# Kernel tuning notes

Measured on AMD Instinct MI355X. Metric: run time of the kernel, lower is better.

## Reference

```python
import jax, jax.numpy as jnp
import numpy as np


def setup_inputs() -> dict:
    key = jax.random.key(0)
    kx, kw = jax.random.split(key)
    B, IN, OUT = 8192, 1024, 4096
    x = jax.random.normal(kx, (B, IN), dtype=jnp.float32)
    # torch.rand -> uniform [0,1)
    weight = jax.random.uniform(kw, (IN, OUT), dtype=jnp.float32)
    return {"x": x, "weight": weight}


def reference(x, weight):
    # Faithful to: (x.unsqueeze(-1) - weight).pow(2).sum(-2)
    # i.e. out[b, o] = sum_i (x[b, i] - weight[i, o])**2
    # Computed via the squared-distance expansion to avoid the
    # (B, in, out) broadcast intermediate:
    x_sq = jnp.sum(x * x, axis=-1, keepdims=True)          # (B, 1)
    w_sq = jnp.sum(weight * weight, axis=0)                # (OUT,)
    cross = jnp.matmul(x, weight)                          # (B, OUT)
    return x_sq - 2.0 * cross + w_sq
```

## Files before the change

kernel.cpp:

```cpp
#include <hip/hip_runtime.h>
#include <cstdint>
#include <cstddef>

#define B_DIM   8192
#define IN_DIM  1024
#define OUT_DIM 4096
#define KT2     (IN_DIM / 64)

typedef __attribute__((ext_vector_type(8)))  int   i32x8;
typedef __attribute__((ext_vector_type(4)))  int   i32x4;
typedef __attribute__((ext_vector_type(16))) float f32x16;

__device__ __forceinline__ void async_copy16(const void* gptr, void* ldsptr) {
    __builtin_amdgcn_global_load_lds(
        (__attribute__((address_space(1))) void*)gptr,
        (__attribute__((address_space(3))) void*)ldsptr,
        16, 0, 0);
}

__device__ __forceinline__ int pack4_fp8(float a, float b, float c, float d) {
    int pk = __builtin_amdgcn_cvt_pk_fp8_f32(a, b, 0, false);
    pk = __builtin_amdgcn_cvt_pk_fp8_f32(c, d, pk, true);
    return pk;
}


__global__ __launch_bounds__(512) void tile_x_kernel(
    const float* __restrict__ x, unsigned char* __restrict__ At,
    float* __restrict__ xsq, float* __restrict__ wsq)
{
    const int t = threadIdx.x;
    const int w = t >> 6;
    const int l = t & 63;
    const int mt = blockIdx.x;
    const int m  = mt * 32 + (l & 31);

    float s = 0.0f;
    #pragma unroll
    for (int c = 0; c < 2; ++c) {
        const int kt2 = c * 8 + w;
        const float* src = x + (size_t)m * IN_DIM + kt2 * 64 + (l >> 5) * 32;
        i32x4 lo, hi;
        #pragma unroll
        for (int j = 0; j < 4; ++j) {
            float4 v = ((const float4*)src)[j];
            s += v.x*v.x + v.y*v.y + v.z*v.z + v.w*v.w;
            lo[j] = pack4_fp8(v.x, v.y, v.z, v.w);
        }
        #pragma unroll
        for (int j = 0; j < 4; ++j) {
            float4 v = ((const float4*)src)[4 + j];
            s += v.x*v.x + v.y*v.y + v.z*v.z + v.w*v.w;
            hi[j] = pack4_fp8(v.x, v.y, v.z, v.w);
        }
        unsigned char* pan = At + ((size_t)mt * KT2 + kt2) * 2048;
        *(i32x4*)(pan + l * 16)        = lo;
        *(i32x4*)(pan + 1024 + l * 16) = hi;
    }
    s += __shfl_down(s, 32, 64);
    __shared__ float red[8][32];
    if (l < 32) red[w][l] = s;
    __syncthreads();
    if (t < 32) {
        float r = 0.0f;
        #pragma unroll
        for (int j = 0; j < 8; ++j) r += red[j][t];
        xsq[mt * 32 + t] = r;
    }

    if (blockIdx.x < 8) wsq[blockIdx.x * 512 + t] = 0.0f;
}

__global__ __launch_bounds__(256) void tile_w_kernel(
    const float* __restrict__ wgt, unsigned char* __restrict__ Bt,
    float* __restrict__ wsq)
{
    __shared__ float tile[256 * 33];
    const int t  = threadIdx.x;
    const int w  = t >> 6;
    const int l  = t & 63;
    const int nt = blockIdx.x;
    const int q  = blockIdx.y;
    const int n0 = nt * 32;

    {
        const int rbase = t >> 2, cg = (t & 3) * 8;
        #pragma unroll
        for (int rep = 0; rep < 4; ++rep) {
            const int r = rbase + rep * 64;
            const float* src = wgt + (size_t)(q * 256 + r) * OUT_DIM + n0 + cg;
            float4 v0 = ((const float4*)src)[0];
            float4 v1 = ((const float4*)src)[1];
            float* d = &tile[r * 33 + cg];
            d[0] = v0.x; d[1] = v0.y; d[2] = v0.z; d[3] = v0.w;
            d[4] = v1.x; d[5] = v1.y; d[6] = v1.z; d[7] = v1.w;
        }
    }
    __syncthreads();

    const int kt2 = q * 4 + w;
    const int n   = l & 31;
    const int kb  = w * 64 + (l >> 5) * 32;
    float s = 0.0f;
    i32x4 lo, hi;
    #pragma unroll
    for (int j4 = 0; j4 < 4; ++j4) {
        float f0 = tile[(kb + j4 * 4 + 0) * 33 + n];
        float f1 = tile[(kb + j4 * 4 + 1) * 33 + n];
        float f2 = tile[(kb + j4 * 4 + 2) * 33 + n];
        float f3 = tile[(kb + j4 * 4 + 3) * 33 + n];
        s += f0*f0 + f1*f1 + f2*f2 + f3*f3;
        lo[j4] = pack4_fp8(f0, f1, f2, f3);
    }
    #pragma unroll
    for (int j4 = 0; j4 < 4; ++j4) {
        float f0 = tile[(kb + 16 + j4 * 4 + 0) * 33 + n];
        float f1 = tile[(kb + 16 + j4 * 4 + 1) * 33 + n];
        float f2 = tile[(kb + 16 + j4 * 4 + 2) * 33 + n];
        float f3 = tile[(kb + 16 + j4 * 4 + 3) * 33 + n];
        s += f0*f0 + f1*f1 + f2*f2 + f3*f3;
        hi[j4] = pack4_fp8(f0, f1, f2, f3);
    }
    unsigned char* pan = Bt + ((size_t)nt * KT2 + kt2) * 2048;
    *(i32x4*)(pan + l * 16)        = lo;
    *(i32x4*)(pan + 1024 + l * 16) = hi;

    s += __shfl_down(s, 32, 64);
    __shared__ float red[4][32];
    if (l < 32) red[w][l] = s;
    __syncthreads();
    if (t < 32) atomicAdd(&wsq[n0 + t], red[0][t] + red[1][t] + red[2][t] + red[3][t]);
}

__global__ __launch_bounds__(256, 2) void rbf_gemm_kernel(
    const unsigned char* __restrict__ At,
    const unsigned char* __restrict__ Bt,
    const float* __restrict__ xsq,
    const float* __restrict__ wsq,
    float* __restrict__ out)
{
    __shared__ __align__(16) unsigned char sm[73728];

    const int t    = threadIdx.x;
    const int w    = t >> 6;
    const int l    = t & 63;
    const int l32  = l & 31;
    const int half = l >> 5;

    const int wg  = blockIdx.y * 64 + blockIdx.x;
    const int swz = (wg & 7) * 128 + (wg >> 3);
    const int bm  = swz >> 4;
    const int bn  = swz & 15;

    f32x16 acc[4][2];
    #pragma unroll
    for (int mi = 0; mi < 4; ++mi)
        #pragma unroll
        for (int ni = 0; ni < 2; ++ni)
            #pragma unroll
            for (int r = 0; r < 16; ++r)
                acc[mi][ni][r] = 0.0f;

    const unsigned char* gaBase  = At + (size_t)(bm * 4 + w)      * (KT2 * 2048);
    const unsigned char* gbBase0 = Bt + (size_t)(bn * 8 + w * 2)  * (KT2 * 2048);
    const unsigned char* gbBase1 = gbBase0 + (size_t)(KT2 * 2048);

    auto stage = [&](int buf, int k) {
        unsigned char* As = sm + buf * 24576;
        unsigned char* Bs = As + 8192;
        const unsigned char* ga  = gaBase  + k * 2048;
        const unsigned char* gb0 = gbBase0 + k * 2048;
        const unsigned char* gb1 = gbBase1 + k * 2048;
        #pragma unroll
        for (int h = 0; h < 2; ++h) {
            async_copy16(ga  + h * 1024 + l * 16, As + w * 2048 + h * 1024);
            async_copy16(gb0 + h * 1024 + l * 16, Bs + (w * 2 + 0) * 2048 + h * 1024);
            async_copy16(gb1 + h * 1024 + l * 16, Bs + (w * 2 + 1) * 2048 + h * 1024);
        }
    };

    auto ldfrag = [&](const unsigned char* base, int p) -> i32x8 {
        i32x4 lo = *(const i32x4*)(base + p * 2048 + l * 16);
        i32x4 hi = *(const i32x4*)(base + p * 2048 + 1024 + l * 16);
        i32x8 r;
        r[0] = lo[0]; r[1] = lo[1]; r[2] = lo[2]; r[3] = lo[3];
        r[4] = hi[0]; r[5] = hi[1]; r[6] = hi[2]; r[7] = hi[3];
        return r;
    };

    stage(0, 0);
    stage(1, 1);

    int cb = 0, sb = 2;
    for (int k = 0; k < 16; ++k) {
        if (k < 15) asm volatile("s_waitcnt vmcnt(6)" ::: "memory");
        else        asm volatile("s_waitcnt vmcnt(0)" ::: "memory");
        __builtin_amdgcn_s_barrier();
        __builtin_amdgcn_sched_barrier(0);

        if (k <= 13) stage(sb, k + 2);

        const unsigned char* As = sm + cb * 24576;
        const unsigned char* Bs = As + 8192;
        i32x8 bf0 = ldfrag(Bs, w * 2 + 0);
        i32x8 bf1 = ldfrag(Bs, w * 2 + 1);
        i32x8 af[4];
        #pragma unroll
        for (int mi = 0; mi < 4; ++mi)
            af[mi] = ldfrag(As, mi);

        __builtin_amdgcn_s_setprio(1);
        #pragma unroll
        for (int mi = 0; mi < 4; ++mi) {
            acc[mi][0] = __builtin_amdgcn_mfma_scale_f32_32x32x64_f8f6f4(
                af[mi], bf0, acc[mi][0],
                0, 0,
                0, 0x7F7F7F7F,
                0, 0x7F7F7F7F);
            acc[mi][1] = __builtin_amdgcn_mfma_scale_f32_32x32x64_f8f6f4(
                af[mi], bf1, acc[mi][1],
                0, 0, 0, 0x7F7F7F7F, 0, 0x7F7F7F7F);
        }
        __builtin_amdgcn_s_setprio(0);

        cb = (cb == 2) ? 0 : cb + 1;
        sb = (sb == 2) ? 0 : sb + 1;
    }

    const int ncol = bn * 256 + w * 64 + l32;
    const float wsn0 = wsq[ncol];
    const float wsn1 = wsq[ncol + 32];
    #pragma unroll
    for (int mi = 0; mi < 4; ++mi) {
        const int mbase = bm * 128 + mi * 32 + 4 * half;
        #pragma unroll
        for (int r2 = 0; r2 < 4; ++r2) {
            #pragma unroll
            for (int r1 = 0; r1 < 4; ++r1) {
                const int m  = mbase + r1 + 8 * r2;
                const float xs = xsq[m];
                float* orow = out + (size_t)m * OUT_DIM + ncol;
                orow[0]  = xs + wsn0 - 2.0f * acc[mi][0][r2 * 4 + r1];
                orow[32] = xs + wsn1 - 2.0f * acc[mi][1][r2 * 4 + r1];
            }
        }
    }
}

extern "C" void kernel_launch(void* const* d_in, const int* in_sizes, int n_in,
                              void* d_out, int out_size, void* d_ws, size_t ws_size,
                              hipStream_t stream)
{
    const float* x   = (const float*)d_in[0];
    const float* wgt = (const float*)d_in[1];
    float* out = (float*)d_out;
    char*  ws  = (char*)d_ws;

    unsigned char* At = (unsigned char*)ws;
    unsigned char* Bt = (unsigned char*)(ws + (size_t)B_DIM * IN_DIM);
    float* xsq = (float*)(ws + (size_t)B_DIM * IN_DIM + (size_t)OUT_DIM * IN_DIM);
    float* wsq = xsq + B_DIM;

    tile_x_kernel<<<B_DIM / 32, 512, 0, stream>>>(x, At, xsq, wsq);
    tile_w_kernel<<<dim3(OUT_DIM / 32, 4), 256, 0, stream>>>(wgt, Bt, wsq);
    rbf_gemm_kernel<<<dim3(64, 16), 256, 0, stream>>>(At, Bt, xsq, wsq, out);
}
```

Before: 194.4 us.

## Merge x and weight quantization kernels and replace atomics with partial sums

Combines the two preprocessing kernels into one launch of 1024 blocks. The first 512 blocks quantize x and the rest quantize the weight. The atomicAdd on the weight norms, and the zeroing it needed, are replaced by per-quarter partial sums that the GEMM epilogue adds up, along with two partial sums for the x norms. This saves one kernel launch and the atomic traffic, and lets the two quantization jobs share the machine. In exchange the epilogue does a few extra loads, and the fused kernel needs the larger LDS tile for every block.

```diff
diff --git a/kernel.cpp b/kernel.cpp
--- a/kernel.cpp
+++ b/kernel.cpp
@@ -25,65 +25,55 @@
 }
 
 
-__global__ __launch_bounds__(512) void tile_x_kernel(
-    const float* __restrict__ x, unsigned char* __restrict__ At,
-    float* __restrict__ xsq, float* __restrict__ wsq)
+__global__ __launch_bounds__(256) void quant_kernel(
+    const float* __restrict__ x, const float* __restrict__ wgt,
+    unsigned char* __restrict__ At, unsigned char* __restrict__ Bt,
+    float* __restrict__ xsq2,
+    float* __restrict__ wsq2)
 {
+    __shared__ float tile[256 * 33];
+    __shared__ float red[4][32];
+
     const int t = threadIdx.x;
     const int w = t >> 6;
     const int l = t & 63;
-    const int mt = blockIdx.x;
-    const int m  = mt * 32 + (l & 31);
-
-    float s = 0.0f;
-    #pragma unroll
-    for (int c = 0; c < 2; ++c) {
-        const int kt2 = c * 8 + w;
-        const float* src = x + (size_t)m * IN_DIM + kt2 * 64 + (l >> 5) * 32;
-        i32x4 lo, hi;
-        #pragma unroll
-        for (int j = 0; j < 4; ++j) {
-            float4 v = ((const float4*)src)[j];
-            s += v.x*v.x + v.y*v.y + v.z*v.z + v.w*v.w;
-            lo[j] = pack4_fp8(v.x, v.y, v.z, v.w);
-        }
-        #pragma unroll
-        for (int j = 0; j < 4; ++j) {
-            float4 v = ((const float4*)src)[4 + j];
-            s += v.x*v.x + v.y*v.y + v.z*v.z + v.w*v.w;
-            hi[j] = pack4_fp8(v.x, v.y, v.z, v.w);
-        }
-        unsigned char* pan = At + ((size_t)mt * KT2 + kt2) * 2048;
-        *(i32x4*)(pan + l * 16)        = lo;
-        *(i32x4*)(pan + 1024 + l * 16) = hi;
-    }
-    s += __shfl_down(s, 32, 64);
-    __shared__ float red[8][32];
-    if (l < 32) red[w][l] = s;
-    __syncthreads();
-    if (t < 32) {
-        float r = 0.0f;
-        #pragma unroll
-        for (int j = 0; j < 8; ++j) r += red[j][t];
-        xsq[mt * 32 + t] = r;
-    }
-
-    if (blockIdx.x < 8) wsq[blockIdx.x * 512 + t] = 0.0f;
-}
-
-__global__ __launch_bounds__(256) void tile_w_kernel(
-    const float* __restrict__ wgt, unsigned char* __restrict__ Bt,
-    float* __restrict__ wsq)
-{
-    __shared__ float tile[256 * 33];
-    const int t  = threadIdx.x;
-    const int w  = t >> 6;
-    const int l  = t & 63;
-    const int nt = blockIdx.x;
-    const int q  = blockIdx.y;
-    const int n0 = nt * 32;
-
-    {
+    const int b = blockIdx.x;
+
+    if (b < 512) {
+        const int mt = b >> 1, kh = b & 1;
+        const int m  = mt * 32 + (l & 31);
+        float s = 0.0f;
+        #pragma unroll
+        for (int p = 0; p < 2; ++p) {
+            const int kt2 = kh * 8 + w * 2 + p;
+            const float* src = x + (size_t)m * IN_DIM + kt2 * 64 + (l >> 5) * 32;
+            i32x4 lo, hi;
+            #pragma unroll
+            for (int j = 0; j < 4; ++j) {
+                float4 v = ((const float4*)src)[j];
+                s += v.x*v.x + v.y*v.y + v.z*v.z + v.w*v.w;
+                lo[j] = pack4_fp8(v.x, v.y, v.z, v.w);
+            }
+            #pragma unroll
+            for (int j = 0; j < 4; ++j) {
+                float4 v = ((const float4*)src)[4 + j];
+                s += v.x*v.x + v.y*v.y + v.z*v.z + v.w*v.w;
+                hi[j] = pack4_fp8(v.x, v.y, v.z, v.w);
+            }
+            unsigned char* pan = At + ((size_t)mt * KT2 + kt2) * 2048;
+            *(i32x4*)(pan + l * 16)        = lo;
+            *(i32x4*)(pan + 1024 + l * 16) = hi;
+        }
+        s += __shfl_down(s, 32, 64);
+        if (l < 32) red[w][l] = s;
+        __syncthreads();
+        if (t < 32)
+            xsq2[kh * B_DIM + mt * 32 + t] =
+                red[0][t] + red[1][t] + red[2][t] + red[3][t];
+    } else {
+        const int idx = b - 512;
+        const int nt = idx & 127, q = idx >> 7, n0 = nt * 32;
+
         const int rbase = t >> 2, cg = (t & 3) * 8;
         #pragma unroll
         for (int rep = 0; rep < 4; ++rep) {
@@ -95,48 +85,49 @@
             d[0] = v0.x; d[1] = v0.y; d[2] = v0.z; d[3] = v0.w;
             d[4] = v1.x; d[5] = v1.y; d[6] = v1.z; d[7] = v1.w;
         }
+        __syncthreads();
+
+        const int kt2 = q * 4 + w;
+        const int n   = l & 31;
+        const int kb  = w * 64 + (l >> 5) * 32;
+        float s = 0.0f;
+        i32x4 lo, hi;
+        #pragma unroll
+        for (int j4 = 0; j4 < 4; ++j4) {
+            float f0 = tile[(kb + j4 * 4 + 0) * 33 + n];
+            float f1 = tile[(kb + j4 * 4 + 1) * 33 + n];
+            float f2 = tile[(kb + j4 * 4 + 2) * 33 + n];
+            float f3 = tile[(kb + j4 * 4 + 3) * 33 + n];
+            s += f0*f0 + f1*f1 + f2*f2 + f3*f3;
+            lo[j4] = pack4_fp8(f0, f1, f2, f3);
+        }
+        #pragma unroll
+        for (int j4 = 0; j4 < 4; ++j4) {
+            float f0 = tile[(kb + 16 + j4 * 4 + 0) * 33 + n];
+            float f1 = tile[(kb + 16 + j4 * 4 + 1) * 33 + n];
+            float f2 = tile[(kb + 16 + j4 * 4 + 2) * 33 + n];
+            float f3 = tile[(kb + 16 + j4 * 4 + 3) * 33 + n];
+            s += f0*f0 + f1*f1 + f2*f2 + f3*f3;
+            hi[j4] = pack4_fp8(f0, f1, f2, f3);
+        }
+        unsigned char* pan = Bt + ((size_t)nt * KT2 + kt2) * 2048;
+        *(i32x4*)(pan + l * 16)        = lo;
+        *(i32x4*)(pan + 1024 + l * 16) = hi;
+
+        s += __shfl_down(s, 32, 64);
+        if (l < 32) red[w][l] = s;
+        __syncthreads();
+        if (t < 32)
+            wsq2[q * OUT_DIM + n0 + t] =
+                red[0][t] + red[1][t] + red[2][t] + red[3][t];
     }
-    __syncthreads();
-
-    const int kt2 = q * 4 + w;
-    const int n   = l & 31;
-    const int kb  = w * 64 + (l >> 5) * 32;
-    float s = 0.0f;
-    i32x4 lo, hi;
-    #pragma unroll
-    for (int j4 = 0; j4 < 4; ++j4) {
-        float f0 = tile[(kb + j4 * 4 + 0) * 33 + n];
-        float f1 = tile[(kb + j4 * 4 + 1) * 33 + n];
-        float f2 = tile[(kb + j4 * 4 + 2) * 33 + n];
-        float f3 = tile[(kb + j4 * 4 + 3) * 33 + n];
-        s += f0*f0 + f1*f1 + f2*f2 + f3*f3;
-        lo[j4] = pack4_fp8(f0, f1, f2, f3);
-    }
-    #pragma unroll
-    for (int j4 = 0; j4 < 4; ++j4) {
-        float f0 = tile[(kb + 16 + j4 * 4 + 0) * 33 + n];
-        float f1 = tile[(kb + 16 + j4 * 4 + 1) * 33 + n];
-        float f2 = tile[(kb + 16 + j4 * 4 + 2) * 33 + n];
-        float f3 = tile[(kb + 16 + j4 * 4 + 3) * 33 + n];
-        s += f0*f0 + f1*f1 + f2*f2 + f3*f3;
-        hi[j4] = pack4_fp8(f0, f1, f2, f3);
-    }
-    unsigned char* pan = Bt + ((size_t)nt * KT2 + kt2) * 2048;
-    *(i32x4*)(pan + l * 16)        = lo;
-    *(i32x4*)(pan + 1024 + l * 16) = hi;
-
-    s += __shfl_down(s, 32, 64);
-    __shared__ float red[4][32];
-    if (l < 32) red[w][l] = s;
-    __syncthreads();
-    if (t < 32) atomicAdd(&wsq[n0 + t], red[0][t] + red[1][t] + red[2][t] + red[3][t]);
 }
 
 __global__ __launch_bounds__(256, 2) void rbf_gemm_kernel(
     const unsigned char* __restrict__ At,
     const unsigned char* __restrict__ Bt,
-    const float* __restrict__ xsq,
-    const float* __restrict__ wsq,
+    const float* __restrict__ xsq2,
+    const float* __restrict__ wsq2,
     float* __restrict__ out)
 {
     __shared__ __align__(16) unsigned char sm[73728];
@@ -228,8 +219,10 @@
     }
 
     const int ncol = bn * 256 + w * 64 + l32;
-    const float wsn0 = wsq[ncol];
-    const float wsn1 = wsq[ncol + 32];
+    const float wsn0 = wsq2[ncol]      + wsq2[OUT_DIM + ncol]
+                     + wsq2[2 * OUT_DIM + ncol]      + wsq2[3 * OUT_DIM + ncol];
+    const float wsn1 = wsq2[ncol + 32] + wsq2[OUT_DIM + ncol + 32]
+                     + wsq2[2 * OUT_DIM + ncol + 32] + wsq2[3 * OUT_DIM + ncol + 32];
     #pragma unroll
     for (int mi = 0; mi < 4; ++mi) {
         const int mbase = bm * 128 + mi * 32 + 4 * half;
@@ -238,7 +231,7 @@
             #pragma unroll
             for (int r1 = 0; r1 < 4; ++r1) {
                 const int m  = mbase + r1 + 8 * r2;
-                const float xs = xsq[m];
+                const float xs = xsq2[m] + xsq2[B_DIM + m];
                 float* orow = out + (size_t)m * OUT_DIM + ncol;
                 orow[0]  = xs + wsn0 - 2.0f * acc[mi][0][r2 * 4 + r1];
                 orow[32] = xs + wsn1 - 2.0f * acc[mi][1][r2 * 4 + r1];
@@ -258,10 +251,9 @@
 
     unsigned char* At = (unsigned char*)ws;
     unsigned char* Bt = (unsigned char*)(ws + (size_t)B_DIM * IN_DIM);
-    float* xsq = (float*)(ws + (size_t)B_DIM * IN_DIM + (size_t)OUT_DIM * IN_DIM);
-    float* wsq = xsq + B_DIM;
-
-    tile_x_kernel<<<B_DIM / 32, 512, 0, stream>>>(x, At, xsq, wsq);
-    tile_w_kernel<<<dim3(OUT_DIM / 32, 4), 256, 0, stream>>>(wgt, Bt, wsq);
-    rbf_gemm_kernel<<<dim3(64, 16), 256, 0, stream>>>(At, Bt, xsq, wsq, out);
-}
+    float* xsq2 = (float*)(ws + (size_t)B_DIM * IN_DIM + (size_t)OUT_DIM * IN_DIM);
+    float* wsq2 = xsq2 + 2 * B_DIM;
+
+    quant_kernel<<<1024, 256, 0, stream>>>(x, wgt, At, Bt, xsq2, wsq2);
+    rbf_gemm_kernel<<<dim3(64, 16), 256, 0, stream>>>(At, Bt, xsq2, wsq2, out);
+}
```

Measured after the change: 191.5 us. About the same (-1.5%).
